# Kernel optimization log

Hardware: AMD Instinct MI355X
Metric: run time of the kernel (lower is better)

The kernel has to match this reference:

```python
import jax, jax.numpy as jnp
import numpy as np

# TT-linear: in_features=1024 -> out_features=4096
IN_DIMS = (8, 8, 4, 4)      # m1..m4, prod = 1024
OUT_DIMS = (8, 8, 8, 8)     # n1..n4, prod = 4096
RANKS = (1, 16, 16, 16, 1)  # r0..r4
IN_FEATURES = 1024
OUT_FEATURES = 4096
BATCH, SEQ = 4, 1024


def _init_core(key, shape):
    # uniform(-1,1)/sqrt(fan_in-ish), matching the original's uniform-style init scale
    fan = shape[0] * shape[1]
    return (2.0 * jax.random.uniform(key, shape, dtype=jnp.float32) - 1.0) / np.sqrt(fan).astype(np.float32)


def setup_inputs() -> dict:
    key = jax.random.key(0)
    ks = jax.random.split(key, 6)
    x = jax.random.normal(ks[0], (BATCH, SEQ, IN_FEATURES), dtype=jnp.float32)
    core0 = _init_core(ks[1], (1, 8, 8, 16))    # [r0, m1, n1, r1]
    core1 = _init_core(ks[2], (16, 8, 8, 16))   # [r1, m2, n2, r2]
    core2 = _init_core(ks[3], (16, 4, 8, 16))   # [r2, m3, n3, r3]
    core3 = _init_core(ks[4], (16, 4, 8, 1))    # [r3, m4, n4, r4]
    bias = (2.0 * jax.random.uniform(ks[5], (OUT_FEATURES,), dtype=jnp.float32) - 1.0) / np.sqrt(OUT_FEATURES).astype(np.float32)
    return {"x": x, "core0": core0, "core1": core1, "core2": core2, "core3": core3, "bias": bias}


def reference(x, core0, core1, core2, core3, bias):
    lead = x.shape[:-1]
    # split the feature axis into TT input factors: [T, m1, m2, m3, m4]
    t = x.reshape((-1,) + IN_DIMS)
    c0 = core0[0]        # [m1, n1, r1]   (boundary rank r0 = 1 squeezed)
    c3 = core3[..., 0]   # [r3, m4, n4]   (boundary rank r4 = 1 squeezed)
    # sequential TT core chain: absorb one m_k, emit one n_k per step
    t = jnp.einsum('tijkl,ixp->tjklxp', t, c0)      # [T, m2,m3,m4, n1, r1]
    t = jnp.einsum('tjklxp,pjyq->tklxyq', t, core1)  # [T, m3,m4, n1,n2, r2]
    t = jnp.einsum('tklxyq,qkzr->tlxyzr', t, core2)  # [T, m4, n1,n2,n3, r3]
    t = jnp.einsum('tlxyzr,rlw->txyzw', t, c3)       # [T, n1,n2,n3,n4]
    y = t.reshape(lead + (OUT_FEATURES,)) + bias
    return y
```

## Files before the change

### kernel.cpp

```cpp
#include <hip/hip_runtime.h>
#include <hip/hip_bf16.h>
#include <cstdint>


typedef __bf16 bf16x8 __attribute__((ext_vector_type(8)));
typedef float f32x4 __attribute__((ext_vector_type(4)));

__device__ __forceinline__ void g2lds16(const void* g, void* l) {
    __builtin_amdgcn_global_load_lds(
        (const __attribute__((address_space(1))) void*)g,
        (__attribute__((address_space(3))) void*)l,
        16, 0, 0);
}

__global__ __launch_bounds__(256) void prep(
    const float* __restrict__ x, __bf16* __restrict__ xb,
    const float* __restrict__ c0, const float* __restrict__ c1,
    const float* __restrict__ c2, const float* __restrict__ c3,
    __bf16* __restrict__ wt) {
    const int b = blockIdx.x;
    const int t = threadIdx.x;
    if (b < 2048) {
        const int i = (b * 256 + t) * 8;
        float4 a0 = *(const float4*)(x + i);
        float4 a1 = *(const float4*)(x + i + 4);
        bf16x8 o;
        o[0] = (__bf16)a0.x; o[1] = (__bf16)a0.y; o[2] = (__bf16)a0.z; o[3] = (__bf16)a0.w;
        o[4] = (__bf16)a1.x; o[5] = (__bf16)a1.y; o[6] = (__bf16)a1.z; o[7] = (__bf16)a1.w;
        *(bf16x8*)(xb + i) = o;
        return;
    }
    __shared__ float t12[4][16];
    __shared__ float t123[4][512];
    __shared__ float c3s[512];
    #pragma unroll
    for (int i = t; i < 512; i += 256) c3s[i] = c3[i];
    const int s = t >> 6;
    const int lane = t & 63;
    const int g = (b - 2048) * 4 + s;
    const int m1 = g >> 9, n1 = (g >> 6) & 7, m2 = (g >> 3) & 7, n2 = g & 7;
    __syncthreads();
    if (lane < 16) {
        const int r2 = lane;
        float sum = 0.f;
        #pragma unroll
        for (int r1 = 0; r1 < 16; ++r1)
            sum += c0[(m1 * 8 + n1) * 16 + r1] * c1[((r1 * 8 + m2) * 8 + n2) * 16 + r2];
        t12[s][r2] = sum;
    }
    __syncthreads();
    #pragma unroll
    for (int idx = lane; idx < 512; idx += 64) {
        const int m3 = idx >> 7, n3 = (idx >> 4) & 7, r3 = idx & 15;
        float sum = 0.f;
        #pragma unroll
        for (int r2 = 0; r2 < 16; ++r2)
            sum += t12[s][r2] * c2[((r2 * 4 + m3) * 8 + n3) * 16 + r3];
        t123[s][(m3 * 8 + n3) * 16 + r3] = sum;
    }
    __syncthreads();
    const int n3 = lane >> 3, n4 = lane & 7;
    const int n = ((n1 * 8 + n2) * 8 + n3) * 8 + n4;
    const int kbase = (m1 * 8 + m2) * 16;
    float v[16];
    #pragma unroll
    for (int e = 0; e < 16; ++e) v[e] = 0.f;
    #pragma unroll
    for (int m3 = 0; m3 < 4; ++m3) {
        #pragma unroll
        for (int r3 = 0; r3 < 16; ++r3) {
            const float tv = t123[s][(m3 * 8 + n3) * 16 + r3];
            #pragma unroll
            for (int m4 = 0; m4 < 4; ++m4)
                v[m3 * 4 + m4] += tv * c3s[(r3 * 4 + m4) * 8 + n4];
        }
    }
    bf16x8 lo, hi;
    #pragma unroll
    for (int e = 0; e < 8; ++e) { lo[e] = (__bf16)v[e]; hi[e] = (__bf16)v[8 + e]; }
    *(bf16x8*)(wt + (size_t)n * 1024 + kbase)     = lo;
    *(bf16x8*)(wt + (size_t)n * 1024 + kbase + 8) = hi;
}

__global__ __launch_bounds__(256) void tt_gemm(
    const __bf16* __restrict__ A, const __bf16* __restrict__ B,
    const float* __restrict__ bias, float* __restrict__ C) {
    constexpr int K = 1024, N = 4096;
    __shared__ __bf16 sA[128 * 64];
    __shared__ __bf16 sB[256 * 64];
    const int t = threadIdx.x;
    const int lane = t & 63;
    const int wave = t >> 6;
    const int wm = (wave >> 1) * 64;
    const int wn = (wave & 1) * 128;
    const int bm = (blockIdx.x >> 4) * 128;
    const int bn = (blockIdx.x & 15) * 256;
    const int l15 = lane & 15, lh = lane >> 4;
    const int swz = l15 & 7;

    f32x4 acc[4][8] = {};

    for (int k0 = 0; k0 < K; k0 += 64) {
        __syncthreads();
        #pragma unroll
        for (int i = 0; i < 4; ++i) {
            const int c = t + i * 256;
            const int r = c >> 3;
            const int gc = (c & 7) ^ (r & 7);
            g2lds16(A + (size_t)(bm + r) * K + k0 + gc * 8, (char*)sA + (size_t)c * 16);
        }
        #pragma unroll
        for (int i = 0; i < 8; ++i) {
            const int c = t + i * 256;
            const int r = c >> 3;
            const int gc = (c & 7) ^ (r & 7);
            g2lds16(B + (size_t)(bn + r) * K + k0 + gc * 8, (char*)sB + (size_t)c * 16);
        }
        asm volatile("s_waitcnt vmcnt(0)" ::: "memory");
        __syncthreads();
        #pragma unroll
        for (int kk = 0; kk < 2; ++kk) {
            const int coff = ((kk * 4 + lh) ^ swz) * 16;
            bf16x8 af[4], bfr[8];
            #pragma unroll
            for (int mi = 0; mi < 4; ++mi)
                af[mi] = *(const bf16x8*)((const char*)sA + (size_t)(wm + mi * 16 + l15) * 128 + coff);
            #pragma unroll
            for (int ni = 0; ni < 8; ++ni)
                bfr[ni] = *(const bf16x8*)((const char*)sB + (size_t)(wn + ni * 16 + l15) * 128 + coff);
            #pragma unroll
            for (int mi = 0; mi < 4; ++mi)
                #pragma unroll
                for (int ni = 0; ni < 8; ++ni)
                    acc[mi][ni] = __builtin_amdgcn_mfma_f32_16x16x32_bf16(
                        af[mi], bfr[ni], acc[mi][ni], 0, 0, 0);
        }
    }

    #pragma unroll
    for (int ni = 0; ni < 8; ++ni) {
        const int col = bn + wn + ni * 16 + l15;
        const float bv = bias[col];
        #pragma unroll
        for (int mi = 0; mi < 4; ++mi) {
            const int row0 = bm + wm + mi * 16 + lh * 4;
            const f32x4 v = acc[mi][ni];
            #pragma unroll
            for (int r = 0; r < 4; ++r)
                C[(size_t)(row0 + r) * N + col] = v[r] + bv;
        }
    }
}

extern "C" void kernel_launch(void* const* d_in, const int* in_sizes, int n_in,
                              void* d_out, int out_size, void* d_ws, size_t ws_size,
                              hipStream_t stream) {
    const float* x    = (const float*)d_in[0];
    const float* c0   = (const float*)d_in[1];
    const float* c1   = (const float*)d_in[2];
    const float* c2   = (const float*)d_in[3];
    const float* c3   = (const float*)d_in[4];
    const float* bias = (const float*)d_in[5];
    float* out = (float*)d_out;

    __bf16* xb = (__bf16*)d_ws;
    __bf16* wt = xb + (size_t)4096 * 1024;

    prep<<<3072, 256, 0, stream>>>(x, xb, c0, c1, c2, c3, wt);
    tt_gemm<<<512, 256, 0, stream>>>(xb, wt, bias, out);
}
```

Measured before the change: 158.8 us.

## Fuse fp32-to-bf16 input conversion into GEMM and switch to 32x32 MFMA tiles

Removes the separate x-to-bf16 conversion pass and instead loads fp32 x directly in the GEMM, converting to bf16 while writing the swizzled LDS tile. The GEMM block tile shrinks from 128x256 to 128x128 (more blocks), and the inner product switches from 16x16x32 to 32x32x16 bf16 MFMA with a matching epilogue. This avoids writing and re-reading an 8 MB bf16 copy of x, but the A-tile now goes through registers with synchronous fp32 loads, and each x row is reread by more column blocks because of the narrower N tile.

```diff
diff --git a/kernel.cpp b/kernel.cpp
--- a/kernel.cpp
+++ b/kernel.cpp
@@ -4,7 +4,7 @@
 
 
 typedef __bf16 bf16x8 __attribute__((ext_vector_type(8)));
-typedef float f32x4 __attribute__((ext_vector_type(4)));
+typedef float f32x16 __attribute__((ext_vector_type(16)));
 
 __device__ __forceinline__ void g2lds16(const void* g, void* l) {
     __builtin_amdgcn_global_load_lds(
@@ -13,40 +13,27 @@
         16, 0, 0);
 }
 
-__global__ __launch_bounds__(256) void prep(
-    const float* __restrict__ x, __bf16* __restrict__ xb,
+__global__ __launch_bounds__(256) void prep_wt(
     const float* __restrict__ c0, const float* __restrict__ c1,
     const float* __restrict__ c2, const float* __restrict__ c3,
     __bf16* __restrict__ wt) {
-    const int b = blockIdx.x;
-    const int t = threadIdx.x;
-    if (b < 2048) {
-        const int i = (b * 256 + t) * 8;
-        float4 a0 = *(const float4*)(x + i);
-        float4 a1 = *(const float4*)(x + i + 4);
-        bf16x8 o;
-        o[0] = (__bf16)a0.x; o[1] = (__bf16)a0.y; o[2] = (__bf16)a0.z; o[3] = (__bf16)a0.w;
-        o[4] = (__bf16)a1.x; o[5] = (__bf16)a1.y; o[6] = (__bf16)a1.z; o[7] = (__bf16)a1.w;
-        *(bf16x8*)(xb + i) = o;
-        return;
-    }
     __shared__ float t12[4][16];
     __shared__ float t123[4][512];
     __shared__ float c3s[512];
+    const int t = threadIdx.x;
     #pragma unroll
     for (int i = t; i < 512; i += 256) c3s[i] = c3[i];
     const int s = t >> 6;
     const int lane = t & 63;
-    const int g = (b - 2048) * 4 + s;
+    const int g = blockIdx.x * 4 + s;
     const int m1 = g >> 9, n1 = (g >> 6) & 7, m2 = (g >> 3) & 7, n2 = g & 7;
     __syncthreads();
     if (lane < 16) {
-        const int r2 = lane;
         float sum = 0.f;
         #pragma unroll
         for (int r1 = 0; r1 < 16; ++r1)
-            sum += c0[(m1 * 8 + n1) * 16 + r1] * c1[((r1 * 8 + m2) * 8 + n2) * 16 + r2];
-        t12[s][r2] = sum;
+            sum += c0[(m1 * 8 + n1) * 16 + r1] * c1[((r1 * 8 + m2) * 8 + n2) * 16 + lane];
+        t12[s][lane] = sum;
     }
     __syncthreads();
     #pragma unroll
@@ -83,22 +70,22 @@
 }
 
 __global__ __launch_bounds__(256) void tt_gemm(
-    const __bf16* __restrict__ A, const __bf16* __restrict__ B,
+    const float* __restrict__ X, const __bf16* __restrict__ B,
     const float* __restrict__ bias, float* __restrict__ C) {
     constexpr int K = 1024, N = 4096;
     __shared__ __bf16 sA[128 * 64];
-    __shared__ __bf16 sB[256 * 64];
+    __shared__ __bf16 sB[128 * 64];
     const int t = threadIdx.x;
     const int lane = t & 63;
     const int wave = t >> 6;
     const int wm = (wave >> 1) * 64;
-    const int wn = (wave & 1) * 128;
-    const int bm = (blockIdx.x >> 4) * 128;
-    const int bn = (blockIdx.x & 15) * 256;
-    const int l15 = lane & 15, lh = lane >> 4;
-    const int swz = l15 & 7;
+    const int wn = (wave & 1) * 64;
+    const int bm = (blockIdx.x >> 5) * 128;
+    const int bn = (blockIdx.x & 31) * 128;
+    const int l31 = lane & 31, l5 = lane >> 5;
+    const int swz = l31 & 7;
 
-    f32x4 acc[4][8] = {};
+    f32x16 acc[2][2] = {};
 
     for (int k0 = 0; k0 < K; k0 += 64) {
         __syncthreads();
@@ -107,47 +94,55 @@
             const int c = t + i * 256;
             const int r = c >> 3;
             const int gc = (c & 7) ^ (r & 7);
-            g2lds16(A + (size_t)(bm + r) * K + k0 + gc * 8, (char*)sA + (size_t)c * 16);
+            g2lds16(B + (size_t)(bn + r) * K + k0 + gc * 8, (char*)sB + (size_t)c * 16);
         }
         #pragma unroll
-        for (int i = 0; i < 8; ++i) {
+        for (int i = 0; i < 4; ++i) {
             const int c = t + i * 256;
             const int r = c >> 3;
-            const int gc = (c & 7) ^ (r & 7);
-            g2lds16(B + (size_t)(bn + r) * K + k0 + gc * 8, (char*)sB + (size_t)c * 16);
+            const int lc = c & 7;
+            const float4* p = (const float4*)(X + (size_t)(bm + r) * K + k0 + lc * 8);
+            float4 a0 = p[0], a1 = p[1];
+            bf16x8 o;
+            o[0] = (__bf16)a0.x; o[1] = (__bf16)a0.y; o[2] = (__bf16)a0.z; o[3] = (__bf16)a0.w;
+            o[4] = (__bf16)a1.x; o[5] = (__bf16)a1.y; o[6] = (__bf16)a1.z; o[7] = (__bf16)a1.w;
+            const int pc = lc ^ (r & 7);
+            *(bf16x8*)((char*)sA + (size_t)(r * 8 + pc) * 16) = o;
         }
         asm volatile("s_waitcnt vmcnt(0)" ::: "memory");
         __syncthreads();
         #pragma unroll
-        for (int kk = 0; kk < 2; ++kk) {
-            const int coff = ((kk * 4 + lh) ^ swz) * 16;
-            bf16x8 af[4], bfr[8];
+        for (int kk = 0; kk < 4; ++kk) {
+            const int coff = ((2 * kk + l5) ^ swz) * 16;
+            bf16x8 af[2], bfr[2];
             #pragma unroll
-            for (int mi = 0; mi < 4; ++mi)
-                af[mi] = *(const bf16x8*)((const char*)sA + (size_t)(wm + mi * 16 + l15) * 128 + coff);
+            for (int mi = 0; mi < 2; ++mi)
+                af[mi] = *(const bf16x8*)((const char*)sA + (size_t)(wm + mi * 32 + l31) * 128 + coff);
             #pragma unroll
-            for (int ni = 0; ni < 8; ++ni)
-                bfr[ni] = *(const bf16x8*)((const char*)sB + (size_t)(wn + ni * 16 + l15) * 128 + coff);
+            for (int ni = 0; ni < 2; ++ni)
+                bfr[ni] = *(const bf16x8*)((const char*)sB + (size_t)(wn + ni * 32 + l31) * 128 + coff);
             #pragma unroll
-            for (int mi = 0; mi < 4; ++mi)
+            for (int mi = 0; mi < 2; ++mi)
                 #pragma unroll
-                for (int ni = 0; ni < 8; ++ni)
-                    acc[mi][ni] = __builtin_amdgcn_mfma_f32_16x16x32_bf16(
+                for (int ni = 0; ni < 2; ++ni)
+                    acc[mi][ni] = __builtin_amdgcn_mfma_f32_32x32x16_bf16(
                         af[mi], bfr[ni], acc[mi][ni], 0, 0, 0);
         }
     }
 
     #pragma unroll
-    for (int ni = 0; ni < 8; ++ni) {
-        const int col = bn + wn + ni * 16 + l15;
+    for (int ni = 0; ni < 2; ++ni) {
+        const int col = bn + wn + ni * 32 + l31;
         const float bv = bias[col];
         #pragma unroll
-        for (int mi = 0; mi < 4; ++mi) {
-            const int row0 = bm + wm + mi * 16 + lh * 4;
-            const f32x4 v = acc[mi][ni];
+        for (int mi = 0; mi < 2; ++mi) {
+            const int row0 = bm + wm + mi * 32 + 4 * l5;
+            const f32x16 v = acc[mi][ni];
             #pragma unroll
-            for (int r = 0; r < 4; ++r)
-                C[(size_t)(row0 + r) * N + col] = v[r] + bv;
+            for (int r = 0; r < 16; ++r) {
+                const int row = row0 + (r & 3) + 8 * (r >> 2);
+                C[(size_t)row * N + col] = v[r] + bv;
+            }
         }
     }
 }
@@ -163,9 +158,8 @@
     const float* bias = (const float*)d_in[5];
     float* out = (float*)d_out;
 
-    __bf16* xb = (__bf16*)d_ws;
-    __bf16* wt = xb + (size_t)4096 * 1024;
+    __bf16* wt = (__bf16*)d_ws;
 
-    prep<<<3072, 256, 0, stream>>>(x, xb, c0, c1, c2, c3, wt);
-    tt_gemm<<<512, 256, 0, stream>>>(xb, wt, bias, out);
+    prep_wt<<<1024, 256, 0, stream>>>(c0, c1, c2, c3, wt);
+    tt_gemm<<<1024, 256, 0, stream>>>(x, wt, bias, out);
 }
```

New measurement: 151.7 us. 1.05x faster.
